# Performance work log

Hardware: AMD Instinct MI355X
Metric: run time of the kernel (lower is better)

The kernel has to match this reference:

```python
import jax, jax.numpy as jnp
import numpy as np

VOCAB = 1_000_000
D = 64
B = 16384
L = 50
PAD_IDX = 0


def setup_inputs() -> dict:
    key = jax.random.key(0)
    k1, k2, k3, k4 = jax.random.split(key, 4)
    idx = jax.random.randint(k1, (B, L), 0, VOCAB, dtype=jnp.int32)
    emb_table = jax.random.normal(k2, (VOCAB, D), dtype=jnp.float32) * 0.02
    # padding_idx row is zero in nn.Embedding.from_pretrained(..., padding_idx=PAD_IDX)
    emb_table = emb_table.at[PAD_IDX].set(0.0)
    attn_weight = jax.random.normal(k3, (1, D), dtype=jnp.float32) * 0.1
    attn_bias = jax.random.normal(k4, (1,), dtype=jnp.float32) * 0.1
    return {"idx": idx, "emb_table": emb_table, "attn_weight": attn_weight, "attn_bias": attn_bias}


def reference(idx, emb_table, attn_weight, attn_bias):
    mask = idx != PAD_IDX                      # [B, L]
    has_real = jnp.any(mask, axis=1)           # [B]
    # rows with no real entries: force mask[i, 0] = True
    mask = mask.at[:, 0].set(jnp.where(has_real, mask[:, 0], True))

    embs = emb_table[idx]                      # [B, L, D] gather
    scores = jnp.einsum('bld,d->bl', embs, attn_weight[0]) + attn_bias[0]  # [B, L]
    scores = jnp.where(mask, scores, -jnp.inf)
    attn = jax.nn.softmax(scores, axis=-1)     # [B, L]
    pooled = jnp.einsum('bl,bld->bd', attn, embs)  # [B, D]
    return jnp.nan_to_num(pooled, nan=0.0)
```

## Files before the change

kernel.cpp:

```cpp
#include <hip/hip_runtime.h>
#include <math.h>

#define VOCAB 1000000
#define D 64
#define BATCH 16384
#define SEQ 50

__global__ __launch_bounds__(256) void attn_pool_kernel(
    const int* __restrict__ idx,
    const float* __restrict__ emb,
    const float* __restrict__ w,
    const float* __restrict__ bias,
    float* __restrict__ out)
{
    const int wave = (int)((blockIdx.x * blockDim.x + threadIdx.x) >> 6);
    const int lane = (int)(threadIdx.x & 63);
    if (wave >= BATCH) return;

    int my_idx = 0;
    if (lane < SEQ) my_idx = idx[wave * SEQ + lane];

    bool valid = (lane < SEQ) && (my_idx != 0);
    unsigned long long ballot = __ballot(valid);
    if (ballot == 0ULL && lane == 0) valid = true;

    const float wl = w[lane];

    float e[SEQ];
    #pragma unroll
    for (int l = 0; l < SEQ; ++l) {
        int il = __builtin_amdgcn_readlane(my_idx, l);
        e[l] = emb[(size_t)il * D + lane];
    }

    float red[SEQ];
    #pragma unroll
    for (int l = 0; l < SEQ; ++l) red[l] = e[l] * wl;

    static const int LENS[7] = {50, 25, 13, 7, 4, 2, 1};
    #pragma unroll
    for (int step = 0; step < 6; ++step) {
        const int m = 1 << step;
        const int len = LENS[step];
        const int npair = LENS[step + 1];
        const bool up = (lane & m) != 0;
        #pragma unroll
        for (int j = 0; j < npair; ++j) {
            float a = red[2 * j];
            float b = (2 * j + 1 < len) ? red[2 * j + 1] : 0.0f;
            float send = up ? a : b;
            float recv = __shfl_xor(send, m);
            red[j] = (up ? b : a) + recv;
        }
    }
    float score = red[0] + bias[0];

    float ms = valid ? score : -INFINITY;
    float m = ms;
    #pragma unroll
    for (int s = 1; s < 64; s <<= 1) m = fmaxf(m, __shfl_xor(m, s));

    float p = valid ? __expf(score - m) : 0.0f;
    float sum = p;
    #pragma unroll
    for (int s = 1; s < 64; s <<= 1) sum += __shfl_xor(sum, s);

    float attn = p / sum;

    float pooled = 0.0f;
    #pragma unroll
    for (int l = 0; l < SEQ; ++l) {
        float a = __uint_as_float(
            __builtin_amdgcn_readlane(__float_as_uint(attn), l));
        pooled = fmaf(a, e[l], pooled);
    }

    out[wave * D + lane] = pooled;
}

extern "C" void kernel_launch(void* const* d_in, const int* in_sizes, int n_in,
                              void* d_out, int out_size, void* d_ws, size_t ws_size,
                              hipStream_t stream) {
    const int*   idx  = (const int*)d_in[0];
    const float* emb  = (const float*)d_in[1];
    const float* w    = (const float*)d_in[2];
    const float* bias = (const float*)d_in[3];
    float* out = (float*)d_out;

    const int threads = 256;
    const int waves_per_block = threads / 64;
    const int blocks = BATCH / waves_per_block;
    attn_pool_kernel<<<blocks, threads, 0, stream>>>(idx, emb, w, bias, out);
}
```

Measured before the change: 37.51 us.

## Split each batch row across two waves with shared-memory softmax and pooling merge

```diff
diff --git a/kernel.cpp b/kernel.cpp
--- a/kernel.cpp
+++ b/kernel.cpp
@@ -1,48 +1,60 @@
 #include <hip/hip_runtime.h>
 #include <math.h>
 
-#define VOCAB 1000000
 #define D 64
 #define BATCH 16384
 #define SEQ 50
+#define HALF 25
 
-__global__ __launch_bounds__(256) void attn_pool_kernel(
+__global__ __launch_bounds__(256, 8) void attn_pool_kernel(
     const int* __restrict__ idx,
     const float* __restrict__ emb,
     const float* __restrict__ w,
     const float* __restrict__ bias,
     float* __restrict__ out)
 {
-    const int wave = (int)((blockIdx.x * blockDim.x + threadIdx.x) >> 6);
+    __shared__ float s_scores[2][64];
+    __shared__ float s_pool[2][64];
+    __shared__ int   s_any[2][2];
+
+    const int wib  = (int)(threadIdx.x >> 6);
     const int lane = (int)(threadIdx.x & 63);
-    if (wave >= BATCH) return;
+    const int rowb = wib >> 1;
+    const int p    = wib & 1;
+    const int row  = (int)blockIdx.x * 2 + rowb;
 
     int my_idx = 0;
-    if (lane < SEQ) my_idx = idx[wave * SEQ + lane];
-
-    bool valid = (lane < SEQ) && (my_idx != 0);
+    if (lane < HALF) my_idx = idx[row * SEQ + p * HALF + lane];
+    bool valid = (lane < HALF) && (my_idx != 0);
     unsigned long long ballot = __ballot(valid);
-    if (ballot == 0ULL && lane == 0) valid = true;
 
     const float wl = w[lane];
 
-    float e[SEQ];
+    float e[HALF];
     #pragma unroll
-    for (int l = 0; l < SEQ; ++l) {
+    for (int l = 0; l < HALF; ++l) {
         int il = __builtin_amdgcn_readlane(my_idx, l);
         e[l] = emb[(size_t)il * D + lane];
     }
 
-    float red[SEQ];
+    float red[13];
+    {
+        const bool up = (lane & 1) != 0;
+        #pragma unroll
+        for (int j = 0; j < 13; ++j) {
+            float a = e[2 * j] * wl;
+            float b = (2 * j + 1 < HALF) ? e[2 * j + 1] * wl : 0.0f;
+            float send = up ? a : b;
+            float recv = __shfl_xor(send, 1);
+            red[j] = (up ? b : a) + recv;
+        }
+    }
+    static const int LENS[6] = {13, 7, 4, 2, 1, 1};
     #pragma unroll
-    for (int l = 0; l < SEQ; ++l) red[l] = e[l] * wl;
-
-    static const int LENS[7] = {50, 25, 13, 7, 4, 2, 1};
-    #pragma unroll
-    for (int step = 0; step < 6; ++step) {
+    for (int step = 1; step < 6; ++step) {
         const int m = 1 << step;
-        const int len = LENS[step];
-        const int npair = LENS[step + 1];
+        const int len = LENS[step - 1];
+        const int npair = LENS[step];
         const bool up = (lane & m) != 0;
         #pragma unroll
         for (int j = 0; j < npair; ++j) {
@@ -55,27 +67,34 @@
     }
     float score = red[0] + bias[0];
 
-    float ms = valid ? score : -INFINITY;
-    float m = ms;
+    if (lane < HALF) s_scores[rowb][p * HALF + lane] = valid ? score : -INFINITY;
+    if (lane == 0)   s_any[rowb][p] = (ballot != 0ULL) ? 1 : 0;
+    __syncthreads();
+
+    float v = (lane < SEQ) ? s_scores[rowb][lane] : -INFINITY;
+    if (lane == 0 && s_any[rowb][0] == 0 && s_any[rowb][1] == 0)
+        v = 0.0f;
+
+    float m = v;
     #pragma unroll
     for (int s = 1; s < 64; s <<= 1) m = fmaxf(m, __shfl_xor(m, s));
-
-    float p = valid ? __expf(score - m) : 0.0f;
-    float sum = p;
+    float pr = __expf(v - m);
+    float sum = pr;
     #pragma unroll
     for (int s = 1; s < 64; s <<= 1) sum += __shfl_xor(sum, s);
-
-    float attn = p / sum;
+    float attn = pr / sum;
 
     float pooled = 0.0f;
     #pragma unroll
-    for (int l = 0; l < SEQ; ++l) {
+    for (int j = 0; j < HALF; ++j) {
         float a = __uint_as_float(
-            __builtin_amdgcn_readlane(__float_as_uint(attn), l));
-        pooled = fmaf(a, e[l], pooled);
+            __builtin_amdgcn_readlane(__float_as_uint(attn), p * HALF + j));
+        pooled = fmaf(a, e[j], pooled);
     }
 
-    out[wave * D + lane] = pooled;
+    if (p == 1) s_pool[rowb][lane] = pooled;
+    __syncthreads();
+    if (p == 0) out[row * D + lane] = pooled + s_pool[rowb][lane];
 }
 
 extern "C" void kernel_launch(void* const* d_in, const int* in_sizes, int n_in,
@@ -88,7 +107,6 @@
     float* out = (float*)d_out;
 
     const int threads = 256;
-    const int waves_per_block = threads / 64;
-    const int blocks = BATCH / waves_per_block;
+    const int blocks = BATCH / 2;
     attn_pool_kernel<<<blocks, threads, 0, stream>>>(idx, emb, w, bias, out);
 }
```

Result: no change. 37.82 us (+0.8%).
